# Kernel tuning notes

Measured on AMD Instinct MI355X. Metric: run time of the kernel, lower is better.

## Reference

```python
import math
import jax, jax.numpy as jnp
import numpy as np

B, T, E = 2, 2048, 2048
NUM_HEADS = 16
H = NUM_HEADS // 2          # differential head pairs = 8
D = E // NUM_HEADS          # head_dim = 128
DEPTH = 12
LAMBDA_INIT = 0.8 - 0.6 * math.exp(-0.3 * DEPTH)
EPS = 1e-5


def setup_inputs() -> dict:
    key = jax.random.key(0)
    ks = jax.random.split(key, 10)
    sc = lambda k, shape, std: jax.random.normal(k, shape, dtype=jnp.float32) * std
    return {
        "x": jax.random.normal(ks[0], (B, T, E), dtype=jnp.float32),
        "Wq": sc(ks[1], (E, E), 0.02),   # [in, out]
        "Wk": sc(ks[2], (E, E), 0.02),   # n_rep == 1 -> k/v proj width = embed_dim
        "Wv": sc(ks[3], (E, E), 0.02),
        "Wo": sc(ks[4], (E, E), 0.02),
        "lambda_q1": sc(ks[5], (D,), 0.1),
        "lambda_k1": sc(ks[6], (D,), 0.1),
        "lambda_q2": sc(ks[7], (D,), 0.1),
        "lambda_k2": sc(ks[8], (D,), 0.1),
        "g": jnp.ones((2 * D,), dtype=jnp.float32),  # RMSNorm weight
    }


def _forward(x, Wq, Wk, Wv, Wo, lq1, lk1, lq2, lk2, g):
    Bz, Tl, _ = x.shape
    # projections; view(bsz, T, 2*H, D).reshape(bsz, T, H, 2, D): adjacent head
    # pairs become the two differential components.
    q = (x @ Wq).reshape(Bz, Tl, H, 2, D)
    k = (x @ Wk).reshape(Bz, Tl, H, 2, D)
    v = (x @ Wv).reshape(Bz, Tl, H, 2 * D)   # value width is 2*head_dim

    scale = D ** -0.5                         # SDPA default scaling
    causal = jnp.tril(jnp.ones((Tl, Tl), dtype=bool))  # is_causal=True

    def attend(qc, kc):
        # qc, kc: [B, T, H, D]
        s = jnp.einsum('bthd,bshd->bhts', qc, kc) * scale
        s = jnp.where(causal, s, -jnp.inf)
        a = jax.nn.softmax(s, axis=-1)
        return jnp.einsum('bhts,bshe->bthe', a, v)  # [B, T, H, 2D]

    # interleaved q/k + repeated v in the single SDPA == two attention maps on full V
    o1 = attend(q[..., 0, :], k[..., 0, :])
    o2 = attend(q[..., 1, :], k[..., 1, :])

    lam = jnp.exp(jnp.sum(lq1 * lk1)) - jnp.exp(jnp.sum(lq2 * lk2)) + LAMBDA_INIT
    o = o1 - lam * o2
    # RMSNorm over last dim (2*head_dim), eps=1e-5, learned weight g
    o = o * jax.lax.rsqrt(jnp.mean(o * o, axis=-1, keepdims=True) + EPS) * g
    o = o * (1.0 - LAMBDA_INIT)
    return o.reshape(Bz, Tl, E) @ Wo


def reference(x, Wq, Wk, Wv, Wo, lambda_q1, lambda_k1, lambda_q2, lambda_k2, g):
    return _forward(x, Wq, Wk, Wv, Wo, lambda_q1, lambda_k1, lambda_q2, lambda_k2, g)
```

## Files before the change

kernel.cpp:

```cpp
#include <hip/hip_runtime.h>
#include <stdint.h>
#include <math.h>


typedef unsigned short u16;
typedef short bf16x8 __attribute__((ext_vector_type(8)));
typedef float f32x4 __attribute__((ext_vector_type(4)));

typedef uint32_t __attribute__((address_space(1))) as1_u32;
typedef uint32_t __attribute__((address_space(3))) as3_u32;

#define LAMBDA_INIT 0.78360576653162453f

__device__ __forceinline__ u16 f2bf(float f) {
  uint32_t u = __float_as_uint(f);
  u += 0x7FFFu + ((u >> 16) & 1u);
  return (u16)(u >> 16);
}
__device__ __forceinline__ float bf2f(u16 v) {
  return __uint_as_float(((uint32_t)v) << 16);
}

__device__ __forceinline__ void async16(u16* lds, const u16* g) {
  __builtin_amdgcn_global_load_lds((const as1_u32*)(uintptr_t)g,
                                   (as3_u32*)(uint32_t)(uintptr_t)lds, 16, 0, 0);
}

__device__ __forceinline__ f32x4 mfma16(bf16x8 a, bf16x8 b, f32x4 c) {
  return __builtin_amdgcn_mfma_f32_16x16x32_bf16(a, b, c, 0, 0, 0);
}


__global__ void cast_x_kernel(const float* __restrict__ x, u16* __restrict__ xb, int n4) {
  int i = blockIdx.x * 256 + threadIdx.x;
  if (i < n4) {
    float4 v = ((const float4*)x)[i];
    ushort4 o;
    o.x = f2bf(v.x); o.y = f2bf(v.y); o.z = f2bf(v.z); o.w = f2bf(v.w);
    ((ushort4*)xb)[i] = o;
  }
}

__global__ void transpose_w_kernel(const float* __restrict__ W, u16* __restrict__ Wt) {
  __shared__ float tile[32][33];
  int tx = threadIdx.x, ty = threadIdx.y;
  int c0 = blockIdx.x * 32, r0 = blockIdx.y * 32;
#pragma unroll
  for (int i = 0; i < 32; i += 8)
    tile[ty + i][tx] = W[(size_t)(r0 + ty + i) * 2048 + c0 + tx];
  __syncthreads();
#pragma unroll
  for (int i = 0; i < 32; i += 8)
    Wt[(size_t)(c0 + ty + i) * 2048 + r0 + tx] = f2bf(tile[tx][ty + i]);
}

__global__ void lam_kernel(const float* __restrict__ lq1, const float* __restrict__ lk1,
                           const float* __restrict__ lq2, const float* __restrict__ lk2,
                           float* __restrict__ out) {
  int L = threadIdx.x;
  float d1 = lq1[L] * lk1[L] + lq1[L + 64] * lk1[L + 64];
  float d2 = lq2[L] * lk2[L] + lq2[L + 64] * lk2[L + 64];
#pragma unroll
  for (int m = 1; m < 64; m <<= 1) {
    d1 += __shfl_xor(d1, m);
    d2 += __shfl_xor(d2, m);
  }
  if (L == 0) out[0] = __expf(d1) - __expf(d2) + LAMBDA_INIT;
}

template <int OUT_BF16>
__global__ __launch_bounds__(256, 2) void gemm_bt_kernel(const u16* __restrict__ A,
                                                         const u16* __restrict__ Bt,
                                                         void* __restrict__ Cout,
                                                         int M, int N, int K) {
  __shared__ __attribute__((aligned(16))) u16 As[128 * 32];
  __shared__ __attribute__((aligned(16))) u16 Bs[128 * 32];
  int t = threadIdx.x;
  int lane = t & 63, w = t >> 6;
  int lr = lane & 15, lq = lane >> 4;
  int m0 = blockIdx.y * 128, n0 = blockIdx.x * 128;
  int wm = (w >> 1) * 64, wn = (w & 1) * 64;
  const u16* Ab = A + (size_t)m0 * K;
  const u16* Bb = Bt + (size_t)n0 * K;
  f32x4 acc[4][4] = {};
  int r0 = t >> 2;
  int kc0 = (t & 3) * 8;

  for (int k0 = 0; k0 < K; k0 += 32) {
    __syncthreads();
    async16(&As[t * 8], Ab + (size_t)r0 * K + k0 + kc0);
    async16(&Bs[t * 8], Bb + (size_t)r0 * K + k0 + kc0);
    async16(&As[(256 + t) * 8], Ab + (size_t)(64 + r0) * K + k0 + kc0);
    async16(&Bs[(256 + t) * 8], Bb + (size_t)(64 + r0) * K + k0 + kc0);
    __syncthreads();
    bf16x8 a[4], b[4];
#pragma unroll
    for (int mi = 0; mi < 4; mi++)
      a[mi] = *(const bf16x8*)&As[(wm + mi * 16 + lr) * 32 + lq * 8];
#pragma unroll
    for (int ni = 0; ni < 4; ni++)
      b[ni] = *(const bf16x8*)&Bs[(wn + ni * 16 + lr) * 32 + lq * 8];
#pragma unroll
    for (int mi = 0; mi < 4; mi++)
#pragma unroll
      for (int ni = 0; ni < 4; ni++)
        acc[mi][ni] = mfma16(a[mi], b[ni], acc[mi][ni]);
  }
#pragma unroll
  for (int mi = 0; mi < 4; mi++) {
#pragma unroll
    for (int ni = 0; ni < 4; ni++) {
#pragma unroll
      for (int r = 0; r < 4; r++) {
        int row = m0 + wm + mi * 16 + lq * 4 + r;
        int col = n0 + wn + ni * 16 + lr;
        if (OUT_BF16)
          ((u16*)Cout)[(size_t)row * N + col] = f2bf(acc[mi][ni][r]);
        else
          ((float*)Cout)[(size_t)row * N + col] = acc[mi][ni][r];
      }
    }
  }
}


struct FlashCtx {
  const u16* Qbase;
  const u16* Kbase;
  const u16* Vbase;
  int t, w, lr, lq;
};

__device__ __forceinline__ void stage_kv(const FlashCtx& cx, int jc,
                                         u16* KsN, u16* VsN) {
#pragma unroll
  for (int i = 0; i < 2; i++) {
    int q = cx.t + i * 256;
    int row = q >> 4, gp = q & 15;
    int gg = (gp & 8) | ((gp & 7) ^ (row & 7));
    async16(&KsN[q * 8], cx.Kbase + (size_t)(jc + row) * 4096 + gg * 8);
  }
#pragma unroll
  for (int i = 0; i < 4; i++) {
    int q = cx.t + i * 256;
    int e = q >> 2, gp = q & 3;
    int gg = gp ^ ((e >> 1) & 3);
    async16(&VsN[q * 8], cx.Vbase + (size_t)e * 4096 + jc + gg * 8);
  }
}

__device__ __forceinline__ void flash_step(const FlashCtx& cx, const bf16x8* qa,
                                           int jc, int njc, int q0,
                                           const u16* KsC, const u16* VsC,
                                           u16* KsN, u16* VsN, u16* PsW,
                                           f32x4* acc, f32x4* lacc, float* m_) {
  __syncthreads();
  if (njc >= 0) stage_kv(cx, njc, KsN, VsN);

  if (jc > q0 + cx.w * 16 + 15) return;
  const float k2 = 0.12753257550036097f;
  int lr = cx.lr, lq = cx.lq;

  f32x4 sacc[2] = {};
#pragma unroll
  for (int ks = 0; ks < 4; ks++) {
#pragma unroll
    for (int ni = 0; ni < 2; ni++) {
      int row = ni * 16 + lr;
      int g = ks * 4 + lq;
      int gp = (g & 8) | ((g & 7) ^ (row & 7));
      bf16x8 kb = *(const bf16x8*)&KsC[row * 128 + gp * 8];
      sacc[ni] = mfma16(qa[ks], kb, sacc[ni]);
    }
  }

  float s2[2][4];
  bool diag = (jc >= q0);
#pragma unroll
  for (int ni = 0; ni < 2; ni++)
#pragma unroll
    for (int r = 0; r < 4; r++) {
      float v = sacc[ni][r] * k2;
      if (diag) {
        int colg = jc + ni * 16 + lr;
        int rowg = q0 + cx.w * 16 + lq * 4 + r;
        if (colg > rowg) v = -INFINITY;
      }
      s2[ni][r] = v;
    }

  float mv = fmaxf(fmaxf(fmaxf(s2[0][0], s2[0][1]), fmaxf(s2[0][2], s2[0][3])),
                   fmaxf(fmaxf(s2[1][0], s2[1][1]), fmaxf(s2[1][2], s2[1][3])));
  mv = fmaxf(mv, __shfl_xor(mv, 1));
  mv = fmaxf(mv, __shfl_xor(mv, 2));
  mv = fmaxf(mv, __shfl_xor(mv, 4));
  mv = fmaxf(mv, __shfl_xor(mv, 8));
  mv = fmaxf(mv, __shfl_xor(mv, 16));
  mv = fmaxf(mv, __shfl_xor(mv, 32));
  float mo = *m_;
  float mn = fmaxf(mo, mv);
  *m_ = mn;
  float a = __builtin_amdgcn_exp2f(mo - mn);

#pragma unroll
  for (int ni = 0; ni < 2; ni++)
#pragma unroll
    for (int r = 0; r < 4; r++) {
      float p = __builtin_amdgcn_exp2f(s2[ni][r] - mn);
      PsW[(lq * 4 + r) * 40 + ni * 16 + lr] = (u16)(__float_as_uint(p) >> 16);
    }

  if (a != 1.0f) {
#pragma unroll
    for (int ei = 0; ei < 16; ei++)
#pragma unroll
      for (int r = 0; r < 4; r++) acc[ei][r] *= a;
#pragma unroll
    for (int r = 0; r < 4; r++) (*lacc)[r] *= a;
  }

  const bf16x8 onesb = {0x3F80, 0x3F80, 0x3F80, 0x3F80, 0x3F80, 0x3F80, 0x3F80, 0x3F80};
  bf16x8 pa = *(const bf16x8*)&PsW[lr * 40 + lq * 8];
#pragma unroll
  for (int ei = 0; ei < 16; ei++) {
    int row = ei * 16 + lr;
    int gp = lq ^ ((row >> 1) & 3);
    bf16x8 vb = *(const bf16x8*)&VsC[row * 32 + gp * 8];
    acc[ei] = mfma16(pa, vb, acc[ei]);
  }
  *lacc = mfma16(pa, onesb, *lacc);
}

__global__ __launch_bounds__(256, 2) void flash_diff_kernel(const u16* __restrict__ QKb,
                                                            const u16* __restrict__ Vt,
                                                            u16* __restrict__ o12b) {
  __shared__ __attribute__((aligned(16))) u16 Ks0[32 * 128];
  __shared__ __attribute__((aligned(16))) u16 Ks1[32 * 128];
  __shared__ __attribute__((aligned(16))) u16 Vs0[256 * 32];
  __shared__ __attribute__((aligned(16))) u16 Vs1[256 * 32];
  __shared__ __attribute__((aligned(16))) u16 Ps[4][16 * 40];

  int t = threadIdx.x;
  FlashCtx cx;
  cx.t = t; cx.w = t >> 6;
  cx.lr = t & 15; cx.lq = (t >> 4) & 3;

  int idx = blockIdx.x;
  int xcd = idx & 7, slot = idx >> 3;
  int pairI = slot & 15, ghi = slot >> 4;
  int g = ghi * 8 + xcd;
  int bh = g >> 1, c = g & 1;
  int b = bh >> 3, h = bh & 7;

  cx.Qbase = QKb + (size_t)b * 2048 * 4096 + h * 256 + c * 128;
  cx.Kbase = cx.Qbase + 2048;
  cx.Vbase = Vt + (size_t)(h * 256) * 4096 + b * 2048;
  u16* Op = o12b + (size_t)c * (4096ull * 2048) + (size_t)b * 2048 * 2048 + h * 256;
  u16* PsW = Ps[cx.w];

  stage_kv(cx, 0, Ks0, Vs0);

#pragma unroll 1
  for (int phase = 0; phase < 2; phase++) {
    int qi = phase ? (31 - pairI) : pairI;
    int q0 = qi * 64;
    int nst = 2 * qi + 2;

    bf16x8 qa[4];
#pragma unroll
    for (int ks = 0; ks < 4; ks++)
      qa[ks] = *(const bf16x8*)&cx.Qbase[(size_t)(q0 + cx.w * 16 + cx.lr) * 4096 +
                                         ks * 32 + cx.lq * 8];

    f32x4 acc[16] = {};
    f32x4 lacc = {};
    float m_ = -INFINITY;

#pragma unroll 1
    for (int jj = 0; jj < nst; jj += 2) {
      int n0c = (jj + 1 < nst) ? (jj + 1) * 32 : -1;
      int n1c;
      if (jj + 2 < nst) n1c = (jj + 2) * 32;
      else n1c = (phase == 0) ? 0 : -1;
      flash_step(cx, qa, jj * 32, n0c, q0, Ks0, Vs0, Ks1, Vs1, PsW, acc, &lacc, &m_);
      flash_step(cx, qa, (jj + 1) * 32, n1c, q0, Ks1, Vs1, Ks0, Vs0, PsW, acc, &lacc, &m_);
    }

#pragma unroll
    for (int r = 0; r < 4; r++) {
      float inv = 1.0f / lacc[r];
      int row = q0 + cx.w * 16 + cx.lq * 4 + r;
#pragma unroll
      for (int ei = 0; ei < 16; ei++)
        Op[(size_t)row * 2048 + ei * 16 + cx.lr] = f2bf(acc[ei][r] * inv);
    }
  }
}

__global__ void combine_kernel(const u16* __restrict__ o12b, const float* __restrict__ lamp,
                               const float* __restrict__ g, u16* __restrict__ ob) {
  __shared__ float red[4];
  int t = threadIdx.x;
  int grp = blockIdx.x;
  size_t idx = (size_t)grp * 256 + t;
  const size_t comp = 4096ull * 2048;
  float lam = lamp[0];
  float v = bf2f(o12b[idx]) - lam * bf2f(o12b[idx + comp]);
  float ss = v * v;
  ss += __shfl_xor(ss, 1);
  ss += __shfl_xor(ss, 2);
  ss += __shfl_xor(ss, 4);
  ss += __shfl_xor(ss, 8);
  ss += __shfl_xor(ss, 16);
  ss += __shfl_xor(ss, 32);
  if ((t & 63) == 0) red[t >> 6] = ss;
  __syncthreads();
  float tot = red[0] + red[1] + red[2] + red[3];
  float scale = rsqrtf(tot * (1.0f / 256.0f) + 1e-5f) * (1.0f - LAMBDA_INIT);
  ob[(size_t)(grp >> 3) * 2048 + (grp & 7) * 256 + t] = f2bf(v * scale * g[t]);
}


extern "C" void kernel_launch(void* const* d_in, const int* in_sizes, int n_in,
                              void* d_out, int out_size, void* d_ws, size_t ws_size,
                              hipStream_t stream) {
  const float* x   = (const float*)d_in[0];
  const float* Wq  = (const float*)d_in[1];
  const float* Wk  = (const float*)d_in[2];
  const float* Wv  = (const float*)d_in[3];
  const float* Wo  = (const float*)d_in[4];
  const float* lq1 = (const float*)d_in[5];
  const float* lk1 = (const float*)d_in[6];
  const float* lq2 = (const float*)d_in[7];
  const float* lk2 = (const float*)d_in[8];
  const float* g   = (const float*)d_in[9];

  char* ws = (char*)d_ws;
  u16* xb    = (u16*)(ws);
  u16* Wtq   = (u16*)(ws + 16777216);
  u16* Wtk   = (u16*)(ws + 25165824);
  u16* Wtv   = (u16*)(ws + 33554432);
  u16* Wto   = (u16*)(ws + 41943040);
  u16* QKb   = (u16*)(ws + 50331648);
  u16* Vt    = (u16*)(ws + 83886080);
  u16* o12b  = (u16*)(ws + 100663296);
  u16* ob    = (u16*)(ws + 134217728);
  float* lamp = (float*)(ws + 150994944);

  cast_x_kernel<<<8192, 256, 0, stream>>>(x, xb, 2097152);
  dim3 tb(32, 8), tg(64, 64);
  transpose_w_kernel<<<tg, tb, 0, stream>>>(Wq, Wtq);
  transpose_w_kernel<<<tg, tb, 0, stream>>>(Wk, Wtk);
  transpose_w_kernel<<<tg, tb, 0, stream>>>(Wv, Wtv);
  transpose_w_kernel<<<tg, tb, 0, stream>>>(Wo, Wto);
  lam_kernel<<<1, 64, 0, stream>>>(lq1, lk1, lq2, lk2, lamp);

  gemm_bt_kernel<1><<<dim3(32, 32), 256, 0, stream>>>(xb, Wtq, QKb, 4096, 4096, 2048);
  gemm_bt_kernel<1><<<dim3(32, 16), 256, 0, stream>>>(Wtv, xb, Vt, 2048, 4096, 2048);

  flash_diff_kernel<<<512, 256, 0, stream>>>(QKb, Vt, o12b);
  combine_kernel<<<32768, 256, 0, stream>>>(o12b, lamp, g, ob);
  gemm_bt_kernel<0><<<dim3(16, 32), 256, 0, stream>>>(ob, Wto, (float*)d_out, 4096, 2048, 2048);
}
```

Measured before the change: 445.3 us.

## Restructure flash attention so each wave owns a V column strip, and merge weight transposes

The flash kernel now splits the 256-wide value dimension across waves. Each wave loads its 64-column V strip straight from global memory into registers instead of staging V through LDS, and the P tiles and per-row rescale factors of all waves are shared through double-buffered LDS. The PV product is software-pipelined one step behind QK/softmax, and the row sums are gathered through LDS before the output is normalised. The four weight-transpose launches are also merged into one launch using gridDim.z. This cuts LDS traffic for V and launch overhead, at the cost of uncached global V loads per wave and extra LDS synchronisation and data exchange.

```diff
diff --git a/kernel.cpp b/kernel.cpp
--- a/kernel.cpp
+++ b/kernel.cpp
@@ -41,8 +41,14 @@
   }
 }
 
-__global__ void transpose_w_kernel(const float* __restrict__ W, u16* __restrict__ Wt) {
+__global__ void transpose_w_kernel(const float* __restrict__ W0, const float* __restrict__ W1,
+                                   const float* __restrict__ W2, const float* __restrict__ W3,
+                                   u16* __restrict__ D0, u16* __restrict__ D1,
+                                   u16* __restrict__ D2, u16* __restrict__ D3) {
   __shared__ float tile[32][33];
+  int z = blockIdx.z;
+  const float* W = (z == 0) ? W0 : (z == 1) ? W1 : (z == 2) ? W2 : W3;
+  u16* Wt = (z == 0) ? D0 : (z == 1) ? D1 : (z == 2) ? D2 : D3;
   int tx = threadIdx.x, ty = threadIdx.y;
   int c0 = blockIdx.x * 32, r0 = blockIdx.y * 32;
 #pragma unroll
@@ -127,12 +133,11 @@
 struct FlashCtx {
   const u16* Qbase;
   const u16* Kbase;
-  const u16* Vbase;
+  const u16* Vstrip;
   int t, w, lr, lq;
 };
 
-__device__ __forceinline__ void stage_kv(const FlashCtx& cx, int jc,
-                                         u16* KsN, u16* VsN) {
+__device__ __forceinline__ void stage_k(const FlashCtx& cx, int jc, u16* KsN) {
 #pragma unroll
   for (int i = 0; i < 2; i++) {
     int q = cx.t + i * 256;
@@ -140,95 +145,117 @@
     int gg = (gp & 8) | ((gp & 7) ^ (row & 7));
     async16(&KsN[q * 8], cx.Kbase + (size_t)(jc + row) * 4096 + gg * 8);
   }
-#pragma unroll
-  for (int i = 0; i < 4; i++) {
-    int q = cx.t + i * 256;
-    int e = q >> 2, gp = q & 3;
-    int gg = gp ^ ((e >> 1) & 3);
-    async16(&VsN[q * 8], cx.Vbase + (size_t)e * 4096 + jc + gg * 8);
-  }
+}
+
+__device__ __forceinline__ void load_v(const FlashCtx& cx, int jc, bf16x8* vb) {
+#pragma unroll
+  for (int et = 0; et < 4; et++)
+    vb[et] = *(const bf16x8*)&cx.Vstrip[(size_t)(et * 16 + cx.lr) * 4096 + jc + cx.lq * 8];
 }
 
 __device__ __forceinline__ void flash_step(const FlashCtx& cx, const bf16x8* qa,
-                                           int jc, int njc, int q0,
-                                           const u16* KsC, const u16* VsC,
-                                           u16* KsN, u16* VsN, u16* PsW,
-                                           f32x4* acc, f32x4* lacc, float* m_) {
+                                           int j, int nst, int q0,
+                                           const u16* KsC, u16* KsN,
+                                           const u16* PsR, u16* PsW,
+                                           const float* AlR, float* AlW,
+                                           const bf16x8* vbU, bf16x8* vbF,
+                                           f32x4 acc[4][4], f32x4* lacc,
+                                           float* m_, float* aprev) {
   __syncthreads();
-  if (njc >= 0) stage_kv(cx, njc, KsN, VsN);
-
-  if (jc > q0 + cx.w * 16 + 15) return;
-  const float k2 = 0.12753257550036097f;
+  int jc = j * 32;
+  if (j + 1 < nst) stage_k(cx, jc + 32, KsN);
+  if (j < nst) load_v(cx, jc, vbF);
+
   int lr = cx.lr, lq = cx.lq;
 
-  f32x4 sacc[2] = {};
-#pragma unroll
-  for (int ks = 0; ks < 4; ks++) {
-#pragma unroll
-    for (int ni = 0; ni < 2; ni++) {
-      int row = ni * 16 + lr;
-      int g = ks * 4 + lq;
-      int gp = (g & 8) | ((g & 7) ^ (row & 7));
-      bf16x8 kb = *(const bf16x8*)&KsC[row * 128 + gp * 8];
-      sacc[ni] = mfma16(qa[ks], kb, sacc[ni]);
-    }
-  }
-
-  float s2[2][4];
-  bool diag = (jc >= q0);
-#pragma unroll
-  for (int ni = 0; ni < 2; ni++)
-#pragma unroll
-    for (int r = 0; r < 4; r++) {
-      float v = sacc[ni][r] * k2;
-      if (diag) {
-        int colg = jc + ni * 16 + lr;
-        int rowg = q0 + cx.w * 16 + lq * 4 + r;
-        if (colg > rowg) v = -INFINITY;
+  if (j >= 1) {
+    f32x4 a4 = *(const f32x4*)AlR;
+    if (a4[0] != 1.0f || a4[1] != 1.0f || a4[2] != 1.0f || a4[3] != 1.0f) {
+#pragma unroll
+      for (int rt = 0; rt < 4; rt++)
+#pragma unroll
+        for (int et = 0; et < 4; et++)
+#pragma unroll
+          for (int r = 0; r < 4; r++) acc[rt][et][r] *= a4[rt];
+    }
+    float aw = *aprev;
+    if (aw != 1.0f)
+#pragma unroll
+      for (int r = 0; r < 4; r++) (*lacc)[r] *= aw;
+    bf16x8 pa[4];
+#pragma unroll
+    for (int rt = 0; rt < 4; rt++)
+      pa[rt] = *(const bf16x8*)&PsR[(rt * 16 + lr) * 40 + lq * 8];
+#pragma unroll
+    for (int rt = 0; rt < 4; rt++)
+#pragma unroll
+      for (int et = 0; et < 4; et++)
+        acc[rt][et] = mfma16(pa[rt], vbU[et], acc[rt][et]);
+    const bf16x8 onesb = {0x3F80, 0x3F80, 0x3F80, 0x3F80,
+                          0x3F80, 0x3F80, 0x3F80, 0x3F80};
+    *lacc = mfma16(pa[cx.w], onesb, *lacc);
+  }
+
+  if (j < nst) {
+    float aj = 1.0f;
+    if (jc <= q0 + cx.w * 16 + 15) {
+      const float k2 = 0.12753257550036097f;
+      f32x4 sacc[2] = {};
+#pragma unroll
+      for (int ks = 0; ks < 4; ks++) {
+#pragma unroll
+        for (int ni = 0; ni < 2; ni++) {
+          int row = ni * 16 + lr;
+          int g = ks * 4 + lq;
+          int gp = (g & 8) | ((g & 7) ^ (row & 7));
+          bf16x8 kb = *(const bf16x8*)&KsC[row * 128 + gp * 8];
+          sacc[ni] = mfma16(qa[ks], kb, sacc[ni]);
+        }
       }
-      s2[ni][r] = v;
-    }
-
-  float mv = fmaxf(fmaxf(fmaxf(s2[0][0], s2[0][1]), fmaxf(s2[0][2], s2[0][3])),
-                   fmaxf(fmaxf(s2[1][0], s2[1][1]), fmaxf(s2[1][2], s2[1][3])));
-  mv = fmaxf(mv, __shfl_xor(mv, 1));
-  mv = fmaxf(mv, __shfl_xor(mv, 2));
-  mv = fmaxf(mv, __shfl_xor(mv, 4));
-  mv = fmaxf(mv, __shfl_xor(mv, 8));
-  mv = fmaxf(mv, __shfl_xor(mv, 16));
-  mv = fmaxf(mv, __shfl_xor(mv, 32));
-  float mo = *m_;
-  float mn = fmaxf(mo, mv);
-  *m_ = mn;
-  float a = __builtin_amdgcn_exp2f(mo - mn);
-
-#pragma unroll
-  for (int ni = 0; ni < 2; ni++)
-#pragma unroll
-    for (int r = 0; r < 4; r++) {
-      float p = __builtin_amdgcn_exp2f(s2[ni][r] - mn);
-      PsW[(lq * 4 + r) * 40 + ni * 16 + lr] = (u16)(__float_as_uint(p) >> 16);
-    }
-
-  if (a != 1.0f) {
-#pragma unroll
-    for (int ei = 0; ei < 16; ei++)
-#pragma unroll
-      for (int r = 0; r < 4; r++) acc[ei][r] *= a;
-#pragma unroll
-    for (int r = 0; r < 4; r++) (*lacc)[r] *= a;
-  }
-
-  const bf16x8 onesb = {0x3F80, 0x3F80, 0x3F80, 0x3F80, 0x3F80, 0x3F80, 0x3F80, 0x3F80};
-  bf16x8 pa = *(const bf16x8*)&PsW[lr * 40 + lq * 8];
-#pragma unroll
-  for (int ei = 0; ei < 16; ei++) {
-    int row = ei * 16 + lr;
-    int gp = lq ^ ((row >> 1) & 3);
-    bf16x8 vb = *(const bf16x8*)&VsC[row * 32 + gp * 8];
-    acc[ei] = mfma16(pa, vb, acc[ei]);
-  }
-  *lacc = mfma16(pa, onesb, *lacc);
+      float s2[2][4];
+      bool diag = (jc >= q0);
+#pragma unroll
+      for (int ni = 0; ni < 2; ni++)
+#pragma unroll
+        for (int r = 0; r < 4; r++) {
+          float v = sacc[ni][r] * k2;
+          if (diag) {
+            int colg = jc + ni * 16 + lr;
+            int rowg = q0 + cx.w * 16 + lq * 4 + r;
+            if (colg > rowg) v = -INFINITY;
+          }
+          s2[ni][r] = v;
+        }
+      float mv = fmaxf(fmaxf(fmaxf(s2[0][0], s2[0][1]), fmaxf(s2[0][2], s2[0][3])),
+                       fmaxf(fmaxf(s2[1][0], s2[1][1]), fmaxf(s2[1][2], s2[1][3])));
+      mv = fmaxf(mv, __shfl_xor(mv, 1));
+      mv = fmaxf(mv, __shfl_xor(mv, 2));
+      mv = fmaxf(mv, __shfl_xor(mv, 4));
+      mv = fmaxf(mv, __shfl_xor(mv, 8));
+      mv = fmaxf(mv, __shfl_xor(mv, 16));
+      mv = fmaxf(mv, __shfl_xor(mv, 32));
+      float mo = *m_;
+      float mn = fmaxf(mo, mv);
+      *m_ = mn;
+      aj = __builtin_amdgcn_exp2f(mo - mn);
+#pragma unroll
+      for (int ni = 0; ni < 2; ni++)
+#pragma unroll
+        for (int r = 0; r < 4; r++) {
+          float p = __builtin_amdgcn_exp2f(s2[ni][r] - mn);
+          PsW[(cx.w * 16 + lq * 4 + r) * 40 + ni * 16 + lr] =
+              (u16)(__float_as_uint(p) >> 16);
+        }
+    } else {
+#pragma unroll
+      for (int ni = 0; ni < 2; ni++)
+#pragma unroll
+        for (int r = 0; r < 4; r++)
+          PsW[(cx.w * 16 + lq * 4 + r) * 40 + ni * 16 + lr] = 0;
+    }
+    if ((cx.t & 63) == 0) AlW[cx.w] = aj;
+    *aprev = aj;
+  }
 }
 
 __global__ __launch_bounds__(256, 2) void flash_diff_kernel(const u16* __restrict__ QKb,
@@ -236,9 +263,11 @@
                                                             u16* __restrict__ o12b) {
   __shared__ __attribute__((aligned(16))) u16 Ks0[32 * 128];
   __shared__ __attribute__((aligned(16))) u16 Ks1[32 * 128];
-  __shared__ __attribute__((aligned(16))) u16 Vs0[256 * 32];
-  __shared__ __attribute__((aligned(16))) u16 Vs1[256 * 32];
-  __shared__ __attribute__((aligned(16))) u16 Ps[4][16 * 40];
+  __shared__ __attribute__((aligned(16))) u16 Ps0[64 * 40];
+  __shared__ __attribute__((aligned(16))) u16 Ps1[64 * 40];
+  __shared__ __attribute__((aligned(16))) float Al0[4];
+  __shared__ __attribute__((aligned(16))) float Al1[4];
+  __shared__ __attribute__((aligned(16))) float lx[64];
 
   int t = threadIdx.x;
   FlashCtx cx;
@@ -254,11 +283,8 @@
 
   cx.Qbase = QKb + (size_t)b * 2048 * 4096 + h * 256 + c * 128;
   cx.Kbase = cx.Qbase + 2048;
-  cx.Vbase = Vt + (size_t)(h * 256) * 4096 + b * 2048;
+  cx.Vstrip = Vt + (size_t)(h * 256 + cx.w * 64) * 4096 + b * 2048;
   u16* Op = o12b + (size_t)c * (4096ull * 2048) + (size_t)b * 2048 * 2048 + h * 256;
-  u16* PsW = Ps[cx.w];
-
-  stage_kv(cx, 0, Ks0, Vs0);
 
 #pragma unroll 1
   for (int phase = 0; phase < 2; phase++) {
@@ -272,28 +298,42 @@
       qa[ks] = *(const bf16x8*)&cx.Qbase[(size_t)(q0 + cx.w * 16 + cx.lr) * 4096 +
                                          ks * 32 + cx.lq * 8];
 
-    f32x4 acc[16] = {};
+    f32x4 acc[4][4] = {};
     f32x4 lacc = {};
-    float m_ = -INFINITY;
+    bf16x8 vbE[4], vbO[4];
+    float m_ = -INFINITY, aprev = 1.0f;
+
+    stage_k(cx, 0, Ks0);
 
 #pragma unroll 1
     for (int jj = 0; jj < nst; jj += 2) {
-      int n0c = (jj + 1 < nst) ? (jj + 1) * 32 : -1;
-      int n1c;
-      if (jj + 2 < nst) n1c = (jj + 2) * 32;
-      else n1c = (phase == 0) ? 0 : -1;
-      flash_step(cx, qa, jj * 32, n0c, q0, Ks0, Vs0, Ks1, Vs1, PsW, acc, &lacc, &m_);
-      flash_step(cx, qa, (jj + 1) * 32, n1c, q0, Ks1, Vs1, Ks0, Vs0, PsW, acc, &lacc, &m_);
-    }
-
-#pragma unroll
-    for (int r = 0; r < 4; r++) {
-      float inv = 1.0f / lacc[r];
-      int row = q0 + cx.w * 16 + cx.lq * 4 + r;
-#pragma unroll
-      for (int ei = 0; ei < 16; ei++)
-        Op[(size_t)row * 2048 + ei * 16 + cx.lr] = f2bf(acc[ei][r] * inv);
-    }
+      flash_step(cx, qa, jj, nst, q0, Ks0, Ks1, Ps1, Ps0, Al1, Al0, vbO, vbE,
+                 acc, &lacc, &m_, &aprev);
+      flash_step(cx, qa, jj + 1, nst, q0, Ks1, Ks0, Ps0, Ps1, Al0, Al1, vbE, vbO,
+                 acc, &lacc, &m_, &aprev);
+    }
+    flash_step(cx, qa, nst, nst, q0, Ks0, Ks1, Ps1, Ps0, Al1, Al0, vbO, vbE,
+               acc, &lacc, &m_, &aprev);
+
+    if (cx.lr == 0) {
+#pragma unroll
+      for (int r = 0; r < 4; r++) lx[cx.w * 16 + cx.lq * 4 + r] = lacc[r];
+    }
+    __syncthreads();
+#pragma unroll
+    for (int rt = 0; rt < 4; rt++) {
+      f32x4 lv = *(const f32x4*)&lx[rt * 16 + cx.lq * 4];
+#pragma unroll
+      for (int r = 0; r < 4; r++) {
+        float inv = 1.0f / lv[r];
+        int row = q0 + rt * 16 + cx.lq * 4 + r;
+#pragma unroll
+        for (int et = 0; et < 4; et++)
+          Op[(size_t)row * 2048 + cx.w * 64 + et * 16 + cx.lr] =
+              f2bf(acc[rt][et][r] * inv);
+      }
+    }
+    __syncthreads();
   }
 }
 
@@ -348,11 +388,8 @@
   float* lamp = (float*)(ws + 150994944);
 
   cast_x_kernel<<<8192, 256, 0, stream>>>(x, xb, 2097152);
-  dim3 tb(32, 8), tg(64, 64);
-  transpose_w_kernel<<<tg, tb, 0, stream>>>(Wq, Wtq);
-  transpose_w_kernel<<<tg, tb, 0, stream>>>(Wk, Wtk);
-  transpose_w_kernel<<<tg, tb, 0, stream>>>(Wv, Wtv);
-  transpose_w_kernel<<<tg, tb, 0, stream>>>(Wo, Wto);
+  transpose_w_kernel<<<dim3(64, 64, 4), dim3(32, 8), 0, stream>>>(
+      Wq, Wk, Wv, Wo, Wtq, Wtk, Wtv, Wto);
   lam_kernel<<<1, 64, 0, stream>>>(lq1, lk1, lq2, lk2, lamp);
 
   gemm_bt_kernel<1><<<dim3(32, 32), 256, 0, stream>>>(xb, Wtq, QKb, 4096, 4096, 2048);
```

Measured after the change: 550.6 us. 1.24x slower.
